# Kernel optimization log

Measured on AMD Instinct MI355X. Metric: run time of the kernel, lower is better.

## Reference

```python
import jax, jax.numpy as jnp
import numpy as np

N_NODES = 400000
MUL_IN1 = 128   # node feature multiplicity per irrep
MUL_IN2 = 4     # potential multiplicity per irrep
MUL_OUT = 4     # charges multiplicity per irrep

# e3nn normalization (component irrep_normalization, element path_normalization):
# fan_in per output irrep = 2 * MUL_IN1 * MUL_IN2 = 1024
# norm(0e out) = sqrt(1/1024) = 1/32 ; norm(1o out) = sqrt(3/1024) = sqrt(3)/32
# wigner-3j: w3j(0,0,0)=1 ; w3j(0,1,1)=w3j(1,0,1)=w3j(1,1,0)=delta/sqrt(3)
_INV32 = 1.0 / 32.0
C000 = _INV32                      # 1/32 * 1
C110 = _INV32 / np.sqrt(3.0)       # 1/32 * 1/sqrt(3)
C011 = _INV32                      # sqrt(3)/32 * 1/sqrt(3)
C101 = _INV32                      # sqrt(3)/32 * 1/sqrt(3)


def setup_inputs() -> dict:
    key = jax.random.key(0)
    k1, k2, k3, k4, k5, k6 = jax.random.split(key, 6)
    node_feat = jax.random.normal(k1, (N_NODES, MUL_IN1 * 1 + MUL_IN1 * 3), dtype=jnp.float32)
    pot_feat = jax.random.normal(k2, (N_NODES, MUL_IN2 * 1 + MUL_IN2 * 3), dtype=jnp.float32)
    wshape = (MUL_IN1, MUL_IN2, MUL_OUT)
    w000 = jax.random.normal(k3, wshape, dtype=jnp.float32)
    w011 = jax.random.normal(k4, wshape, dtype=jnp.float32)
    w101 = jax.random.normal(k5, wshape, dtype=jnp.float32)
    w110 = jax.random.normal(k6, wshape, dtype=jnp.float32)
    return {"node_feat": node_feat, "pot_feat": pot_feat,
            "w000": w000, "w011": w011, "w101": w101, "w110": w110}


def _fctp(node_feat, pot_feat, w000, w011, w101, w110):
    n = node_feat.shape[0]
    x0 = node_feat[:, :MUL_IN1]                              # [n, 128]   0e
    x1 = node_feat[:, MUL_IN1:].reshape(n, MUL_IN1, 3)       # [n, 128,3] 1o
    y0 = pot_feat[:, :MUL_IN2]                               # [n, 4]     0e
    y1 = pot_feat[:, MUL_IN2:].reshape(n, MUL_IN2, 3)        # [n, 4, 3]  1o
    # output 0e: (0e x 0e) + (1o . 1o)
    out0 = (C000 * jnp.einsum('nu,nv,uvw->nw', x0, y0, w000)
            + C110 * jnp.einsum('nui,nvi,uvw->nw', x1, y1, w110))   # [n, 4]
    # output 1o: (0e x 1o) + (1o x 0e)
    out1 = (C011 * jnp.einsum('nu,nvk,uvw->nwk', x0, y1, w011)
            + C101 * jnp.einsum('nuk,nv,uvw->nwk', x1, y0, w101))   # [n, 4, 3]
    return jnp.concatenate([out0, out1.reshape(n, MUL_OUT * 3)], axis=1)  # [n, 16]


def reference(node_feat, pot_feat, w000, w011, w101, w110):
    mpoles = 0.01 * _fctp(node_feat, pot_feat, w000, w011, w101, w110)
    # zero_charges=True: zero the first component, keep [:, 1:]
    zeroed = mpoles.at[:, 0].set(0.0)
    return zeroed
```

## Files before the change

kernel.cpp:

```cpp
#include <hip/hip_runtime.h>


#define NBLK 128
#define BLOCK 256
#define NITER 8
#define X0_STRIDE 17
#define X1_STRIDE 49
#define X0_REGION (NBLK * X0_STRIDE)
#define BUF_DW (NBLK * (X0_STRIDE + X1_STRIDE))

__global__ __launch_bounds__(BLOCK, 2)
void fctp_kernel(const float* __restrict__ nf, const float* __restrict__ pf,
                 const float* __restrict__ w000, const float* __restrict__ w011,
                 const float* __restrict__ w101, const float* __restrict__ w110,
                 float* __restrict__ out)
{
    __shared__ float lds[2 * BUF_DW];

    const int t  = threadIdx.x;
    const int n0 = blockIdx.x * NBLK;
    const int m  = t & (NBLK - 1);
    const int roleS = __builtin_amdgcn_readfirstlane(t >> 7);

    const float4* pf4 = (const float4*)(pf + (size_t)(n0 + m) * 16);
    float4 ya = pf4[0], yb = pf4[1], yc = pf4[2], yd = pf4[3];
    const float y00 = ya.x, y01 = ya.y, y02 = ya.z, y03 = ya.w;
    float y1v[4][3] = {{yb.x, yb.y, yb.z},
                       {yb.w, yc.x, yc.y},
                       {yc.z, yc.w, yd.x},
                       {yd.y, yd.z, yd.w}};

    int mm0[2], jj0[2], mm1[6], jj1[6];
#pragma unroll
    for (int s = 0; s < 2; ++s) { int idx = t + BLOCK * s; mm0[s] = idx >> 2; jj0[s] = idx & 3; }
#pragma unroll
    for (int s = 0; s < 6; ++s) { int idx = t + BLOCK * s; mm1[s] = idx / 12; jj1[s] = idx % 12; }

    float4 rx0[2], rx1[6];
    auto load_iter = [&](int k) {
#pragma unroll
        for (int s = 0; s < 2; ++s)
            rx0[s] = *(const float4*)(nf + (size_t)(n0 + mm0[s]) * 512 + 16 * k + 4 * jj0[s]);
#pragma unroll
        for (int s = 0; s < 6; ++s)
            rx1[s] = *(const float4*)(nf + (size_t)(n0 + mm1[s]) * 512 + 128 + 48 * k + 4 * jj1[s]);
    };
    auto store_iter = [&](int k) {
        float* b = lds + (k & 1) * BUF_DW;
#pragma unroll
        for (int s = 0; s < 2; ++s) {
            float* p = b + mm0[s] * X0_STRIDE + 4 * jj0[s];
            p[0] = rx0[s].x; p[1] = rx0[s].y; p[2] = rx0[s].z; p[3] = rx0[s].w;
        }
#pragma unroll
        for (int s = 0; s < 6; ++s) {
            float* p = b + X0_REGION + mm1[s] * X1_STRIDE + 4 * jj1[s];
            p[0] = rx1[s].x; p[1] = rx1[s].y; p[2] = rx1[s].z; p[3] = rx1[s].w;
        }
    };

    float o0[4]    = {0.f, 0.f, 0.f, 0.f};
    float o1[4][3] = {{0.f,0.f,0.f},{0.f,0.f,0.f},{0.f,0.f,0.f},{0.f,0.f,0.f}};

    load_iter(0);
    store_iter(0);

#pragma unroll 1
    for (int k = 0; k < NITER; ++k) {
        __syncthreads();
        if (k + 1 < NITER) load_iter(k + 1);
        const float* buf = lds + (k & 1) * BUF_DW;

        if (roleS == 0) {
            const float* xp = buf + m * X0_STRIDE;
#pragma unroll
            for (int j = 0; j < 16; ++j) {
                const int u = 16 * k + j;
                const float xv = xp[j];
                const float* wa = w000 + u * 16;
                const float* wb = w011 + u * 16;
#pragma unroll
                for (int w = 0; w < 4; ++w) {
                    float bb = y00 * wa[w];
                    bb = fmaf(y01, wa[4 + w], bb);
                    bb = fmaf(y02, wa[8 + w], bb);
                    bb = fmaf(y03, wa[12 + w], bb);
                    o0[w] = fmaf(xv, bb, o0[w]);
                }
#pragma unroll
                for (int w = 0; w < 4; ++w) {
#pragma unroll
                    for (int c = 0; c < 3; ++c) {
                        float bb = y1v[0][c] * wb[w];
                        bb = fmaf(y1v[1][c], wb[4 + w], bb);
                        bb = fmaf(y1v[2][c], wb[8 + w], bb);
                        bb = fmaf(y1v[3][c], wb[12 + w], bb);
                        o1[w][c] = fmaf(xv, bb, o1[w][c]);
                    }
                }
            }
        } else {
            const float* xp = buf + X0_REGION + m * X1_STRIDE;
#pragma unroll
            for (int j = 0; j < 16; ++j) {
                const int u = 16 * k + j;
                const float xa = xp[3 * j], xb = xp[3 * j + 1], xc = xp[3 * j + 2];
                const float* wc = w110 + u * 16;
                const float* wd = w101 + u * 16;
#pragma unroll
                for (int w = 0; w < 4; ++w) {
                    float t0 = y1v[0][0] * wc[w];
                    t0 = fmaf(y1v[1][0], wc[4 + w], t0);
                    t0 = fmaf(y1v[2][0], wc[8 + w], t0);
                    t0 = fmaf(y1v[3][0], wc[12 + w], t0);
                    o0[w] = fmaf(xa, t0, o0[w]);
                    float t1 = y1v[0][1] * wc[w];
                    t1 = fmaf(y1v[1][1], wc[4 + w], t1);
                    t1 = fmaf(y1v[2][1], wc[8 + w], t1);
                    t1 = fmaf(y1v[3][1], wc[12 + w], t1);
                    o0[w] = fmaf(xb, t1, o0[w]);
                    float t2 = y1v[0][2] * wc[w];
                    t2 = fmaf(y1v[1][2], wc[4 + w], t2);
                    t2 = fmaf(y1v[2][2], wc[8 + w], t2);
                    t2 = fmaf(y1v[3][2], wc[12 + w], t2);
                    o0[w] = fmaf(xc, t2, o0[w]);
                    float ss = y00 * wd[w];
                    ss = fmaf(y01, wd[4 + w], ss);
                    ss = fmaf(y02, wd[8 + w], ss);
                    ss = fmaf(y03, wd[12 + w], ss);
                    o1[w][0] = fmaf(xa, ss, o1[w][0]);
                    o1[w][1] = fmaf(xb, ss, o1[w][1]);
                    o1[w][2] = fmaf(xc, ss, o1[w][2]);
                }
            }
        }
        if (k + 1 < NITER) store_iter(k + 1);
    }

    const float K000 = 0.01f / 32.0f;
    const float K011 = 0.01f / 32.0f;
    const float K101 = 0.01f / 32.0f;
    const float K110 = 1.8042195912175807e-4f;

    if (roleS != 0) {
        float* rp = lds + m * X0_STRIDE;
#pragma unroll
        for (int w = 0; w < 4; ++w) rp[w] = K110 * o0[w];
#pragma unroll
        for (int w = 0; w < 4; ++w) {
            rp[4 + 3 * w + 0] = K101 * o1[w][0];
            rp[4 + 3 * w + 1] = K101 * o1[w][1];
            rp[4 + 3 * w + 2] = K101 * o1[w][2];
        }
    }
    __syncthreads();
    if (roleS == 0) {
        const float* rp = lds + m * X0_STRIDE;
        float r[16];
        r[0] = 0.0f;
#pragma unroll
        for (int w = 1; w < 4; ++w) r[w] = fmaf(K000, o0[w], rp[w]);
#pragma unroll
        for (int w = 0; w < 4; ++w) {
#pragma unroll
            for (int c = 0; c < 3; ++c) {
                const int idx = 4 + 3 * w + c;
                r[idx] = fmaf(K011, o1[w][c], rp[idx]);
            }
        }
        float4 v0 = {r[0],  r[1],  r[2],  r[3]};
        float4 v1 = {r[4],  r[5],  r[6],  r[7]};
        float4 v2 = {r[8],  r[9],  r[10], r[11]};
        float4 v3 = {r[12], r[13], r[14], r[15]};
        float4* op = (float4*)(out + (size_t)(n0 + m) * 16);
        op[0] = v0; op[1] = v1; op[2] = v2; op[3] = v3;
    }
}

extern "C" void kernel_launch(void* const* d_in, const int* in_sizes, int n_in,
                              void* d_out, int out_size, void* d_ws, size_t ws_size,
                              hipStream_t stream)
{
    const float* nf   = (const float*)d_in[0];
    const float* pf   = (const float*)d_in[1];
    const float* w000 = (const float*)d_in[2];
    const float* w011 = (const float*)d_in[3];
    const float* w101 = (const float*)d_in[4];
    const float* w110 = (const float*)d_in[5];
    float* out = (float*)d_out;

    const int n_nodes = in_sizes[0] / 512;
    fctp_kernel<<<n_nodes / NBLK, BLOCK, 0, stream>>>(nf, pf, w000, w011, w101, w110, out);
}
```

Baseline: 1.830 ms.

## Stream node features into LDS with direct global_load_lds DMA and smaller chunks

Replaces the register-staged global→LDS copy with `__builtin_amdgcn_global_load_lds` transfers. These write node-feature chunks straight into a packed double-buffered LDS layout. The per-iteration chunk is halved (8 irreps over 16 iterations), which shrinks LDS use, and launch bounds are raised to 4 blocks per CU to increase occupancy. The compute loops now read LDS with float4 vector loads. In exchange, the padded strides are removed, which may bring back bank conflicts. It also relies on the barrier correctly ordering the asynchronous LDS writes.

```diff
diff --git a/kernel.cpp b/kernel.cpp
--- a/kernel.cpp
+++ b/kernel.cpp
@@ -3,13 +3,15 @@
 
 #define NBLK 128
 #define BLOCK 256
-#define NITER 8
-#define X0_STRIDE 17
-#define X1_STRIDE 49
-#define X0_REGION (NBLK * X0_STRIDE)
-#define BUF_DW (NBLK * (X0_STRIDE + X1_STRIDE))
-
-__global__ __launch_bounds__(BLOCK, 2)
+#define NITER 16
+#define CHUNK 8
+#define X0_DW 1024
+#define BUF_DW 4096
+
+#define GLOBAL_ASP const __attribute__((address_space(1))) void*
+#define LDS_ASP __attribute__((address_space(3))) void*
+
+__global__ __launch_bounds__(BLOCK, 4)
 void fctp_kernel(const float* __restrict__ nf, const float* __restrict__ pf,
                  const float* __restrict__ w000, const float* __restrict__ w011,
                  const float* __restrict__ w101, const float* __restrict__ w110,
@@ -21,6 +23,8 @@
     const int n0 = blockIdx.x * NBLK;
     const int m  = t & (NBLK - 1);
     const int roleS = __builtin_amdgcn_readfirstlane(t >> 7);
+    const int W  = __builtin_amdgcn_readfirstlane(t >> 6);
+    const int l  = t & 63;
 
     const float4* pf4 = (const float4*)(pf + (size_t)(n0 + m) * 16);
     float4 ya = pf4[0], yb = pf4[1], yc = pf4[2], yd = pf4[3];
@@ -30,53 +34,51 @@
                        {yc.z, yc.w, yd.x},
                        {yd.y, yd.z, yd.w}};
 
-    int mm0[2], jj0[2], mm1[6], jj1[6];
-#pragma unroll
-    for (int s = 0; s < 2; ++s) { int idx = t + BLOCK * s; mm0[s] = idx >> 2; jj0[s] = idx & 3; }
-#pragma unroll
-    for (int s = 0; s < 6; ++s) { int idx = t + BLOCK * s; mm1[s] = idx / 12; jj1[s] = idx % 12; }
-
-    float4 rx0[2], rx1[6];
-    auto load_iter = [&](int k) {
-#pragma unroll
-        for (int s = 0; s < 2; ++s)
-            rx0[s] = *(const float4*)(nf + (size_t)(n0 + mm0[s]) * 512 + 16 * k + 4 * jj0[s]);
-#pragma unroll
-        for (int s = 0; s < 6; ++s)
-            rx1[s] = *(const float4*)(nf + (size_t)(n0 + mm1[s]) * 512 + 128 + 48 * k + 4 * jj1[s]);
-    };
-    auto store_iter = [&](int k) {
-        float* b = lds + (k & 1) * BUF_DW;
-#pragma unroll
-        for (int s = 0; s < 2; ++s) {
-            float* p = b + mm0[s] * X0_STRIDE + 4 * jj0[s];
-            p[0] = rx0[s].x; p[1] = rx0[s].y; p[2] = rx0[s].z; p[3] = rx0[s].w;
-        }
-#pragma unroll
-        for (int s = 0; s < 6; ++s) {
-            float* p = b + X0_REGION + mm1[s] * X1_STRIDE + 4 * jj1[s];
-            p[0] = rx1[s].x; p[1] = rx1[s].y; p[2] = rx1[s].z; p[3] = rx1[s].w;
-        }
+    const int  m0dma = W * 32 + (l >> 1);
+    const int  b0dma = l & 1;
+    const float* gx0 = nf + (size_t)(n0 + m0dma) * 512 + 4 * b0dma;
+
+    const float* gx1[3];
+    int d1[3];
+#pragma unroll
+    for (int s = 0; s < 3; ++s) {
+        const int r  = (W * 3 + s) * 256 + 4 * l;
+        const int mm = r / 24;
+        const int gg = (r - 24 * mm) >> 2;
+        gx1[s] = nf + (size_t)(n0 + mm) * 512 + 128 + 4 * gg;
+        d1[s]  = X0_DW + (W * 3 + s) * 256;
+    }
+    const int d0 = W * 256;
+
+    auto dma = [&](int buf, int k) {
+        __builtin_amdgcn_global_load_lds((GLOBAL_ASP)(gx0 + 8 * k),
+                                         (LDS_ASP)(lds + buf * BUF_DW + d0), 16, 0, 0);
+#pragma unroll
+        for (int s = 0; s < 3; ++s)
+            __builtin_amdgcn_global_load_lds((GLOBAL_ASP)(gx1[s] + 24 * k),
+                                             (LDS_ASP)(lds + buf * BUF_DW + d1[s]), 16, 0, 0);
     };
 
     float o0[4]    = {0.f, 0.f, 0.f, 0.f};
     float o1[4][3] = {{0.f,0.f,0.f},{0.f,0.f,0.f},{0.f,0.f,0.f},{0.f,0.f,0.f}};
 
-    load_iter(0);
-    store_iter(0);
+    dma(0, 0);
 
 #pragma unroll 1
     for (int k = 0; k < NITER; ++k) {
         __syncthreads();
-        if (k + 1 < NITER) load_iter(k + 1);
+        if (k + 1 < NITER) dma((k + 1) & 1, k + 1);
         const float* buf = lds + (k & 1) * BUF_DW;
 
         if (roleS == 0) {
-            const float* xp = buf + m * X0_STRIDE;
-#pragma unroll
-            for (int j = 0; j < 16; ++j) {
-                const int u = 16 * k + j;
-                const float xv = xp[j];
+            const float* xp = buf + m * 8;
+            const float4 va = *(const float4*)xp;
+            const float4 vb = *(const float4*)(xp + 4);
+            float xs[8] = {va.x, va.y, va.z, va.w, vb.x, vb.y, vb.z, vb.w};
+#pragma unroll
+            for (int j = 0; j < CHUNK; ++j) {
+                const int u = CHUNK * k + j;
+                const float xv = xs[j];
                 const float* wa = w000 + u * 16;
                 const float* wb = w011 + u * 16;
 #pragma unroll
@@ -100,11 +102,20 @@
                 }
             }
         } else {
-            const float* xp = buf + X0_REGION + m * X1_STRIDE;
-#pragma unroll
-            for (int j = 0; j < 16; ++j) {
-                const int u = 16 * k + j;
-                const float xa = xp[3 * j], xb = xp[3 * j + 1], xc = xp[3 * j + 2];
+            const float* xq = buf + X0_DW + m * 24;
+            const float4 q0 = *(const float4*)(xq);
+            const float4 q1 = *(const float4*)(xq + 4);
+            const float4 q2 = *(const float4*)(xq + 8);
+            const float4 q3 = *(const float4*)(xq + 12);
+            const float4 q4 = *(const float4*)(xq + 16);
+            const float4 q5 = *(const float4*)(xq + 20);
+            float xf[24] = {q0.x,q0.y,q0.z,q0.w, q1.x,q1.y,q1.z,q1.w,
+                            q2.x,q2.y,q2.z,q2.w, q3.x,q3.y,q3.z,q3.w,
+                            q4.x,q4.y,q4.z,q4.w, q5.x,q5.y,q5.z,q5.w};
+#pragma unroll
+            for (int j = 0; j < CHUNK; ++j) {
+                const int u = CHUNK * k + j;
+                const float xa = xf[3 * j], xb = xf[3 * j + 1], xc = xf[3 * j + 2];
                 const float* wc = w110 + u * 16;
                 const float* wd = w101 + u * 16;
 #pragma unroll
@@ -134,7 +145,6 @@
                 }
             }
         }
-        if (k + 1 < NITER) store_iter(k + 1);
     }
 
     const float K000 = 0.01f / 32.0f;
@@ -143,7 +153,7 @@
     const float K110 = 1.8042195912175807e-4f;
 
     if (roleS != 0) {
-        float* rp = lds + m * X0_STRIDE;
+        float* rp = lds + m * 17;
 #pragma unroll
         for (int w = 0; w < 4; ++w) rp[w] = K110 * o0[w];
 #pragma unroll
@@ -155,7 +165,7 @@
     }
     __syncthreads();
     if (roleS == 0) {
-        const float* rp = lds + m * X0_STRIDE;
+        const float* rp = lds + m * 17;
         float r[16];
         r[0] = 0.0f;
 #pragma unroll
```

After: 1.709 ms. -6.6%, faster.
